# Kernel optimization log

Hardware: AMD Instinct MI355X
Metric: run time of the kernel (lower is better)

Reference implementation:

```python
import jax, jax.numpy as jnp
import numpy as np

N_NODES = 100000
N_EDGES = 1600000
IN_DIM = 16
HEADS = 4
CH = 32  # per-head channels


def _gat_layer(x, src, dst, W, att_src, att_dst, b, concat):
    """PyG GATConv (eval mode): gather -> edge logits -> segment softmax -> scatter-agg."""
    n = x.shape[0]
    H, C = att_src.shape
    h = (x @ W).reshape(n, H, C)                      # [N,H,C]
    a_src = jnp.einsum('nhc,hc->nh', h, att_src)      # [N,H]
    a_dst = jnp.einsum('nhc,hc->nh', h, att_dst)
    e = jax.nn.leaky_relu(a_src[src] + a_dst[dst], negative_slope=0.2)  # [E,H]
    m = jax.ops.segment_max(e, dst, num_segments=n)   # stable softmax per dst node
    p = jnp.exp(e - m[dst])
    s = jax.ops.segment_sum(p, dst, num_segments=n)
    alpha = p / s[dst]                                 # [E,H]
    out = jax.ops.segment_sum(alpha[:, :, None] * h[src], dst, num_segments=n)  # [N,H,C]
    out = out.reshape(n, H * C) if concat else out.mean(axis=1)
    return out + b


def setup_inputs() -> dict:
    key = jax.random.key(0)
    ks = jax.random.split(key, 20)
    d1 = HEADS * CH  # 128

    def gl(k, shape):  # glorot-ish
        fan = sum(shape[-2:]) if len(shape) > 1 else shape[-1]
        return jax.random.normal(k, shape, dtype=jnp.float32) * (2.0 / fan) ** 0.5

    return {
        'x': jax.random.normal(ks[0], (N_NODES, IN_DIM), dtype=jnp.float32),
        'edge_index': jax.random.randint(ks[1], (2, N_EDGES), 0, N_NODES, dtype=jnp.int32),
        'W1': gl(ks[2], (IN_DIM, d1)), 'aS1': gl(ks[3], (HEADS, CH)), 'aD1': gl(ks[4], (HEADS, CH)), 'b1': jnp.zeros((d1,), jnp.float32),
        'W2': gl(ks[5], (d1, d1)),     'aS2': gl(ks[6], (HEADS, CH)), 'aD2': gl(ks[7], (HEADS, CH)), 'b2': jnp.zeros((d1,), jnp.float32),
        'W3': gl(ks[8], (d1, CH)),     'aS3': gl(ks[9], (1, CH)),     'aD3': gl(ks[10], (1, CH)),    'b3': jnp.zeros((CH,), jnp.float32),
        'reg_w': gl(ks[11], (CH, 1)), 'reg_b': jnp.zeros((1,), jnp.float32),
        'cls_w': gl(ks[12], (CH, 1)), 'cls_b': jnp.zeros((1,), jnp.float32),
    }


def reference(x, edge_index, W1, aS1, aD1, b1, W2, aS2, aD2, b2, W3, aS3, aD3, b3, reg_w, reg_b, cls_w, cls_b):
    n = x.shape[0]
    loops = jnp.arange(n, dtype=edge_index.dtype)  # PyG add_self_loops=True
    src = jnp.concatenate([edge_index[0], loops])
    dst = jnp.concatenate([edge_index[1], loops])

    h = jax.nn.elu(_gat_layer(x, src, dst, W1, aS1, aD1, b1, concat=True))
    h = jax.nn.elu(_gat_layer(h, src, dst, W2, aS2, aD2, b2, concat=True)) + h
    h = jax.nn.elu(_gat_layer(h, src, dst, W3, aS3, aD3, b3, concat=False))

    reg = (h @ reg_w + reg_b).squeeze(-1)
    cls = (h @ cls_w + cls_b).squeeze(-1)
    return reg, cls
```

## Files before the change

kernel.cpp:

```cpp
#include <hip/hip_runtime.h>
#include <hip/hip_bf16.h>
#include <cstdint>

#define CDIV(a,b) (((a)+(b)-1)/(b))

__device__ __forceinline__ float lrelu(float x){ return x > 0.f ? x : 0.2f*x; }
__device__ __forceinline__ float eluf(float x){ return x > 0.f ? x : __expf(x) - 1.f; }
__device__ __forceinline__ unsigned short f2bf(float f){
  unsigned x = __float_as_uint(f);
  return (unsigned short)((x + 0x7fffu + ((x >> 16) & 1u)) >> 16);
}
__device__ __forceinline__ float bf2f(unsigned short u){ return __uint_as_float(((unsigned)u) << 16); }

__global__ void hist_k(const int* __restrict__ ei, int* __restrict__ deg, int ne, int etot){
  int e = blockIdx.x*256 + threadIdx.x;
  if (e >= etot) return;
  int d = (e < ne) ? ei[ne + e] : (e - ne);
  atomicAdd(&deg[d], 1);
}

constexpr int SCHUNK = 2048;

__global__ __launch_bounds__(256) void scan_part_k(const int* __restrict__ in, int* __restrict__ out,
                                                   int* __restrict__ blksum, int n){
  __shared__ int lds[256];
  int base = blockIdx.x*SCHUNK + threadIdx.x*8;
  int v[8]; int tsum = 0;
  #pragma unroll
  for (int k=0;k<8;k++){ int idx=base+k; int x=(idx<n)?in[idx]:0; v[k]=tsum; tsum+=x; }
  lds[threadIdx.x]=tsum; __syncthreads();
  for (int off=1; off<256; off<<=1){
    int y = (threadIdx.x>= (unsigned)off)? lds[threadIdx.x-off]:0;
    __syncthreads();
    lds[threadIdx.x]+=y;
    __syncthreads();
  }
  int excl = lds[threadIdx.x] - tsum;
  #pragma unroll
  for (int k=0;k<8;k++){ int idx=base+k; if(idx<n) out[idx]=excl+v[k]; }
  if (threadIdx.x==255) blksum[blockIdx.x]=lds[255];
}

__global__ __launch_bounds__(256) void scan_top_k(int* __restrict__ blksum, int nb){
  __shared__ int lds[256];
  int x = ((int)threadIdx.x<nb)? blksum[threadIdx.x]:0;
  lds[threadIdx.x]=x; __syncthreads();
  for (int off=1; off<256; off<<=1){
    int y=(threadIdx.x>=(unsigned)off)?lds[threadIdx.x-off]:0;
    __syncthreads();
    lds[threadIdx.x]+=y;
    __syncthreads();
  }
  if ((int)threadIdx.x<nb) blksum[threadIdx.x]=lds[threadIdx.x]-x;
}

__global__ void scan_add_k(int* __restrict__ rowstart, const int* __restrict__ blksum,
                           int* __restrict__ cursor, int n, int etot){
  int i = blockIdx.x*256+threadIdx.x;
  if (i<n){ int r = rowstart[i]+blksum[i/SCHUNK]; rowstart[i]=r; cursor[i]=r; }
  if (i==0) rowstart[n]=etot;
}

__global__ void scatter_k(const int* __restrict__ ei, int* __restrict__ cursor,
                          int* __restrict__ edge_src, int ne, int etot, int lo, int hi){
  int e = blockIdx.x*256+threadIdx.x;
  if (e>=etot) return;
  int s,d;
  if (e<ne){ s=ei[e]; d=ei[ne+e]; } else { s=e-ne; d=s; }
  if (d < lo || d >= hi) return;
  int p = atomicAdd(&cursor[d],1);
  edge_src[p]=s;
}

template<int K, int KC, int M, int NPT, int H>
__global__ __launch_bounds__(256) void gemm_att_k(const float* __restrict__ X, const float* __restrict__ W,
    const float* __restrict__ attS, const float* __restrict__ attD,
    unsigned short* __restrict__ Hb, float* __restrict__ asrc, float* __restrict__ adst, int n){
  constexpr int CG = M/8;
  constexpr int NG = 256/CG;
  constexpr int NT = NG*NPT;
  constexpr int XS = KC + 4;
  __shared__ float Xl[NT*XS];
  __shared__ float Wl[KC*M];

  const int tid = threadIdx.x;
  const int cg  = tid % CG;
  const int nd  = tid / CG;
  const int base = blockIdx.x * NT;

  float acc[NPT][8];
  #pragma unroll
  for (int j=0;j<NPT;++j)
    #pragma unroll
    for (int c=0;c<8;++c) acc[j][c]=0.f;

  for (int kc0 = 0; kc0 < K; kc0 += KC){
    __syncthreads();
    for (int i = tid; i < NT*KC/4; i += 256){
      int node = i / (KC/4);
      int k4   = i % (KC/4);
      float4 v = make_float4(0.f,0.f,0.f,0.f);
      if (base + node < n) v = *(const float4*)&X[(size_t)(base+node)*K + kc0 + k4*4];
      *(float4*)&Xl[node*XS + k4*4] = v;
    }
    const float* Wsrc = W + (size_t)kc0*M;
    for (int i = tid; i < KC*M/4; i += 256)
      *(float4*)&Wl[i*4] = *(const float4*)&Wsrc[i*4];
    __syncthreads();

    #pragma unroll 4
    for (int k4 = 0; k4 < KC/4; ++k4){
      float4 xv[NPT];
      #pragma unroll
      for (int j=0;j<NPT;++j) xv[j] = *(const float4*)&Xl[(nd + NG*j)*XS + k4*4];
      #pragma unroll
      for (int kk=0;kk<4;++kk){
        float4 w0 = *(const float4*)&Wl[(k4*4+kk)*M + cg*8];
        float4 w1 = *(const float4*)&Wl[(k4*4+kk)*M + cg*8 + 4];
        #pragma unroll
        for (int j=0;j<NPT;++j){
          float x = ((const float*)&xv[j])[kk];
          acc[j][0] += x*w0.x; acc[j][1] += x*w0.y; acc[j][2] += x*w0.z; acc[j][3] += x*w0.w;
          acc[j][4] += x*w1.x; acc[j][5] += x*w1.y; acc[j][6] += x*w1.z; acc[j][7] += x*w1.w;
        }
      }
    }
  }

  const int c0 = cg*8;
  float s0=attS[c0],s1=attS[c0+1],s2=attS[c0+2],s3=attS[c0+3],
        s4=attS[c0+4],s5=attS[c0+5],s6=attS[c0+6],s7=attS[c0+7];
  float d0=attD[c0],d1=attD[c0+1],d2=attD[c0+2],d3=attD[c0+3],
        d4=attD[c0+4],d5=attD[c0+5],d6=attD[c0+6],d7=attD[c0+7];
  #pragma unroll
  for (int j=0;j<NPT;++j){
    int node = base + nd + NG*j;
    float vs = acc[j][0]*s0+acc[j][1]*s1+acc[j][2]*s2+acc[j][3]*s3
             + acc[j][4]*s4+acc[j][5]*s5+acc[j][6]*s6+acc[j][7]*s7;
    float vd = acc[j][0]*d0+acc[j][1]*d1+acc[j][2]*d2+acc[j][3]*d3
             + acc[j][4]*d4+acc[j][5]*d5+acc[j][6]*d6+acc[j][7]*d7;
    vs += __shfl_xor(vs,1); vs += __shfl_xor(vs,2);
    vd += __shfl_xor(vd,1); vd += __shfl_xor(vd,2);
    if (node < n){
      uint4 pk;
      pk.x = (unsigned)f2bf(acc[j][0]) | ((unsigned)f2bf(acc[j][1])<<16);
      pk.y = (unsigned)f2bf(acc[j][2]) | ((unsigned)f2bf(acc[j][3])<<16);
      pk.z = (unsigned)f2bf(acc[j][4]) | ((unsigned)f2bf(acc[j][5])<<16);
      pk.w = (unsigned)f2bf(acc[j][6]) | ((unsigned)f2bf(acc[j][7])<<16);
      *(uint4*)&Hb[(size_t)node*M + c0] = pk;
      if ((cg & 3)==0){
        int head = cg>>2;
        asrc[(size_t)node*H+head]=vs;
        adst[(size_t)node*H+head]=vd;
      }
    }
  }
}

template<bool RES>
__global__ __launch_bounds__(256, 4) void agg4_k(const unsigned short* __restrict__ Hb, const float* __restrict__ asrc,
    const float* __restrict__ adst, const int* __restrict__ rowstart, const int* __restrict__ esrc,
    const float* __restrict__ bias, float* __restrict__ out, int n){
  __shared__ float alphaS[4][64][4];
  const int w    = threadIdx.x >> 6;
  const int lane = threadIdx.x & 63;
  int wid  = (int)((blockIdx.x*256 + threadIdx.x) >> 6);
  if (wid >= n) return;
  wid = __builtin_amdgcn_readfirstlane(wid);
  const int rs = rowstart[wid], re = rowstart[wid+1];
  const int deg = re - rs;
  const float4 adv = *(const float4*)&adst[(size_t)wid*4];
  const int head = lane >> 4;

  float acc0 = 0.f, acc1 = 0.f;

  if (deg <= 64){
    int s = 0;
    float l0=-1e30f,l1=-1e30f,l2=-1e30f,l3=-1e30f;
    if (lane < deg){
      s = esrc[rs + lane];
      float4 a4 = *(const float4*)&asrc[(size_t)s*4];
      l0 = lrelu(a4.x+adv.x); l1 = lrelu(a4.y+adv.y);
      l2 = lrelu(a4.z+adv.z); l3 = lrelu(a4.w+adv.w);
    }
    float m0=l0,m1=l1,m2=l2,m3=l3;
    #pragma unroll
    for (int mask=32; mask; mask>>=1){
      m0=fmaxf(m0,__shfl_xor(m0,mask)); m1=fmaxf(m1,__shfl_xor(m1,mask));
      m2=fmaxf(m2,__shfl_xor(m2,mask)); m3=fmaxf(m3,__shfl_xor(m3,mask));
    }
    float e0=__expf(l0-m0), e1=__expf(l1-m1), e2=__expf(l2-m2), e3=__expf(l3-m3);
    float s0=e0,s1=e1,s2=e2,s3=e3;
    #pragma unroll
    for (int mask=32; mask; mask>>=1){
      s0+=__shfl_xor(s0,mask); s1+=__shfl_xor(s1,mask);
      s2+=__shfl_xor(s2,mask); s3+=__shfl_xor(s3,mask);
    }
    *(float4*)&alphaS[w][lane][0] = make_float4(e0/s0, e1/s1, e2/s2, e3/s3);

    int jj = 0;
    for (; jj+8 <= deg; jj += 8){
      int sj0 = __builtin_amdgcn_readlane(s, jj+0);
      int sj1 = __builtin_amdgcn_readlane(s, jj+1);
      int sj2 = __builtin_amdgcn_readlane(s, jj+2);
      int sj3 = __builtin_amdgcn_readlane(s, jj+3);
      int sj4 = __builtin_amdgcn_readlane(s, jj+4);
      int sj5 = __builtin_amdgcn_readlane(s, jj+5);
      int sj6 = __builtin_amdgcn_readlane(s, jj+6);
      int sj7 = __builtin_amdgcn_readlane(s, jj+7);
      ushort2 h0 = ((const ushort2*)(Hb + (size_t)sj0*128))[lane];
      ushort2 h1 = ((const ushort2*)(Hb + (size_t)sj1*128))[lane];
      ushort2 h2 = ((const ushort2*)(Hb + (size_t)sj2*128))[lane];
      ushort2 h3 = ((const ushort2*)(Hb + (size_t)sj3*128))[lane];
      ushort2 h4 = ((const ushort2*)(Hb + (size_t)sj4*128))[lane];
      ushort2 h5 = ((const ushort2*)(Hb + (size_t)sj5*128))[lane];
      ushort2 h6 = ((const ushort2*)(Hb + (size_t)sj6*128))[lane];
      ushort2 h7 = ((const ushort2*)(Hb + (size_t)sj7*128))[lane];
      float a0 = alphaS[w][jj+0][head];
      float a1 = alphaS[w][jj+1][head];
      float a2 = alphaS[w][jj+2][head];
      float a3 = alphaS[w][jj+3][head];
      float a4 = alphaS[w][jj+4][head];
      float a5 = alphaS[w][jj+5][head];
      float a6 = alphaS[w][jj+6][head];
      float a7 = alphaS[w][jj+7][head];
      acc0 += a0*bf2f(h0.x) + a1*bf2f(h1.x) + a2*bf2f(h2.x) + a3*bf2f(h3.x)
            + a4*bf2f(h4.x) + a5*bf2f(h5.x) + a6*bf2f(h6.x) + a7*bf2f(h7.x);
      acc1 += a0*bf2f(h0.y) + a1*bf2f(h1.y) + a2*bf2f(h2.y) + a3*bf2f(h3.y)
            + a4*bf2f(h4.y) + a5*bf2f(h5.y) + a6*bf2f(h6.y) + a7*bf2f(h7.y);
    }
    for (; jj+4 <= deg; jj += 4){
      int sj0 = __builtin_amdgcn_readlane(s, jj+0);
      int sj1 = __builtin_amdgcn_readlane(s, jj+1);
      int sj2 = __builtin_amdgcn_readlane(s, jj+2);
      int sj3 = __builtin_amdgcn_readlane(s, jj+3);
      ushort2 h0 = ((const ushort2*)(Hb + (size_t)sj0*128))[lane];
      ushort2 h1 = ((const ushort2*)(Hb + (size_t)sj1*128))[lane];
      ushort2 h2 = ((const ushort2*)(Hb + (size_t)sj2*128))[lane];
      ushort2 h3 = ((const ushort2*)(Hb + (size_t)sj3*128))[lane];
      float a0 = alphaS[w][jj+0][head];
      float a1 = alphaS[w][jj+1][head];
      float a2 = alphaS[w][jj+2][head];
      float a3 = alphaS[w][jj+3][head];
      acc0 += a0*bf2f(h0.x) + a1*bf2f(h1.x) + a2*bf2f(h2.x) + a3*bf2f(h3.x);
      acc1 += a0*bf2f(h0.y) + a1*bf2f(h1.y) + a2*bf2f(h2.y) + a3*bf2f(h3.y);
    }
    for (; jj < deg; ++jj){
      int sj = __builtin_amdgcn_readlane(s, jj);
      ushort2 hv = ((const ushort2*)(Hb + (size_t)sj*128))[lane];
      float a = alphaS[w][jj][head];
      acc0 += a*bf2f(hv.x);
      acc1 += a*bf2f(hv.y);
    }
  } else {
    float adl[4] = {adv.x, adv.y, adv.z, adv.w};
    float m[4] = {-1e30f,-1e30f,-1e30f,-1e30f};
    for (int i = rs + lane; i < re; i += 64){
      int s = esrc[i];
      float4 a4 = *(const float4*)&asrc[(size_t)s*4];
      m[0]=fmaxf(m[0], lrelu(a4.x+adl[0]));
      m[1]=fmaxf(m[1], lrelu(a4.y+adl[1]));
      m[2]=fmaxf(m[2], lrelu(a4.z+adl[2]));
      m[3]=fmaxf(m[3], lrelu(a4.w+adl[3]));
    }
    #pragma unroll
    for (int h=0; h<4; ++h){
      #pragma unroll
      for (int mask=32; mask; mask>>=1) m[h] = fmaxf(m[h], __shfl_xor(m[h], mask));
    }
    float sum[4] = {0.f,0.f,0.f,0.f};
    for (int i = rs + lane; i < re; i += 64){
      int s = esrc[i];
      float4 a4 = *(const float4*)&asrc[(size_t)s*4];
      sum[0]+=__expf(lrelu(a4.x+adl[0])-m[0]);
      sum[1]+=__expf(lrelu(a4.y+adl[1])-m[1]);
      sum[2]+=__expf(lrelu(a4.z+adl[2])-m[2]);
      sum[3]+=__expf(lrelu(a4.w+adl[3])-m[3]);
    }
    #pragma unroll
    for (int h=0; h<4; ++h){
      #pragma unroll
      for (int mask=32; mask; mask>>=1) sum[h]+=__shfl_xor(sum[h],mask);
    }
    const float ad = adl[head], mm = m[head], iv = 1.f/sum[head];
    int i = rs;
    for (; i+4 <= re; i += 4){
      int s0=esrc[i], s1=esrc[i+1], s2=esrc[i+2], s3=esrc[i+3];
      float a0 = asrc[(size_t)s0*4+head];
      float a1 = asrc[(size_t)s1*4+head];
      float a2 = asrc[(size_t)s2*4+head];
      float a3 = asrc[(size_t)s3*4+head];
      ushort2 h0 = ((const ushort2*)(Hb + (size_t)s0*128))[lane];
      ushort2 h1 = ((const ushort2*)(Hb + (size_t)s1*128))[lane];
      ushort2 h2 = ((const ushort2*)(Hb + (size_t)s2*128))[lane];
      ushort2 h3 = ((const ushort2*)(Hb + (size_t)s3*128))[lane];
      float e0=__expf(lrelu(a0+ad)-mm)*iv;
      float e1=__expf(lrelu(a1+ad)-mm)*iv;
      float e2=__expf(lrelu(a2+ad)-mm)*iv;
      float e3=__expf(lrelu(a3+ad)-mm)*iv;
      acc0 += e0*bf2f(h0.x) + e1*bf2f(h1.x) + e2*bf2f(h2.x) + e3*bf2f(h3.x);
      acc1 += e0*bf2f(h0.y) + e1*bf2f(h1.y) + e2*bf2f(h2.y) + e3*bf2f(h3.y);
    }
    for (; i < re; ++i){
      int s = esrc[i];
      float a = asrc[(size_t)s*4+head];
      ushort2 hv = ((const ushort2*)(Hb + (size_t)s*128))[lane];
      float e = __expf(lrelu(a+ad)-mm)*iv;
      acc0 += e*bf2f(hv.x);
      acc1 += e*bf2f(hv.y);
    }
  }

  float2 bv = *(const float2*)&bias[2*lane];
  float v0 = eluf(acc0 + bv.x);
  float v1 = eluf(acc1 + bv.y);
  if (RES){
    float2 rv = *(const float2*)&out[(size_t)wid*128 + 2*lane];
    v0 += rv.x; v1 += rv.y;
  }
  *(float2*)&out[(size_t)wid*128 + 2*lane] = make_float2(v0, v1);
}

__global__ __launch_bounds__(256) void agg1_heads_k(const unsigned short* __restrict__ Hb, const float* __restrict__ asrc,
    const float* __restrict__ adst, const int* __restrict__ rowstart, const int* __restrict__ esrc,
    const float* __restrict__ bias,
    const float* __restrict__ rw, const float* __restrict__ rb,
    const float* __restrict__ cw, const float* __restrict__ cb,
    float* __restrict__ out, int n){
  __shared__ float alphaS[4][64];
  const int w    = threadIdx.x >> 6;
  const int lane = threadIdx.x & 63;
  int wid  = (int)((blockIdx.x*256 + threadIdx.x) >> 6);
  if (wid >= n) return;
  wid = __builtin_amdgcn_readfirstlane(wid);
  const int rs = rowstart[wid], re = rowstart[wid+1];
  const int deg = re - rs;
  const float adl = adst[wid];
  const int q = lane >> 4, c2 = lane & 15;

  float acc0 = 0.f, acc1 = 0.f;

  if (deg <= 64){
    int s = 0;
    float l = -1e30f;
    if (lane < deg){
      s = esrc[rs + lane];
      l = lrelu(asrc[s]+adl);
    }
    float m = l;
    #pragma unroll
    for (int mask=32; mask; mask>>=1) m = fmaxf(m, __shfl_xor(m, mask));
    float e = __expf(l-m);
    float sum = e;
    #pragma unroll
    for (int mask=32; mask; mask>>=1) sum += __shfl_xor(sum, mask);
    alphaS[w][lane] = e/sum;

    for (int jj = 0; jj < deg; jj += 4){
      int idx = jj + q;
      int sj = __shfl(s, idx);
      float av = (idx < 64) ? alphaS[w][idx] : 0.f;
      ushort2 hv = ((const ushort2*)(Hb + (size_t)sj*32))[c2];
      acc0 += av*bf2f(hv.x);
      acc1 += av*bf2f(hv.y);
    }
  } else {
    float m = -1e30f;
    for (int i = rs + lane; i < re; i += 64) m = fmaxf(m, lrelu(asrc[esrc[i]]+adl));
    #pragma unroll
    for (int mask=32; mask; mask>>=1) m = fmaxf(m, __shfl_xor(m, mask));
    float sum = 0.f;
    for (int i = rs + lane; i < re; i += 64) sum += __expf(lrelu(asrc[esrc[i]]+adl)-m);
    #pragma unroll
    for (int mask=32; mask; mask>>=1) sum += __shfl_xor(sum, mask);
    const float iv = 1.f/sum;
    for (int i = rs; i < re; i += 4){
      int eidx = i + q;
      if (eidx < re){
        int s = esrc[eidx];
        float a = asrc[s];
        float e = __expf(lrelu(a+adl)-m)*iv;
        ushort2 hv = ((const ushort2*)(Hb + (size_t)s*32))[c2];
        acc0 += e*bf2f(hv.x);
        acc1 += e*bf2f(hv.y);
      }
    }
  }

  acc0 += __shfl_xor(acc0,16); acc0 += __shfl_xor(acc0,32);
  acc1 += __shfl_xor(acc1,16); acc1 += __shfl_xor(acc1,32);

  float2 bv = *(const float2*)&bias[2*c2];
  float v0 = eluf(acc0 + bv.x);
  float v1 = eluf(acc1 + bv.y);
  float r  = v0*rw[2*c2] + v1*rw[2*c2+1];
  float cl = v0*cw[2*c2] + v1*cw[2*c2+1];
  #pragma unroll
  for (int mask=1; mask<16; mask<<=1){ r += __shfl_xor(r, mask); cl += __shfl_xor(cl, mask); }
  if (lane == 0){
    out[wid]     = r  + rb[0];
    out[n + wid] = cl + cb[0];
  }
}

extern "C" void kernel_launch(void* const* d_in, const int* in_sizes, int n_in,
                              void* d_out, int out_size, void* d_ws, size_t ws_size,
                              hipStream_t stream){
  const float* x   = (const float*)d_in[0];
  const int*   ei  = (const int*)d_in[1];
  const float* W1  = (const float*)d_in[2];
  const float* aS1 = (const float*)d_in[3];
  const float* aD1 = (const float*)d_in[4];
  const float* b1  = (const float*)d_in[5];
  const float* W2  = (const float*)d_in[6];
  const float* aS2 = (const float*)d_in[7];
  const float* aD2 = (const float*)d_in[8];
  const float* b2  = (const float*)d_in[9];
  const float* W3  = (const float*)d_in[10];
  const float* aS3 = (const float*)d_in[11];
  const float* aD3 = (const float*)d_in[12];
  const float* b3  = (const float*)d_in[13];
  const float* rw  = (const float*)d_in[14];
  const float* rb  = (const float*)d_in[15];
  const float* cw  = (const float*)d_in[16];
  const float* cb  = (const float*)d_in[17];
  float* out = (float*)d_out;

  const int n    = in_sizes[0] / 16;
  const int ne   = in_sizes[1] / 2;
  const int etot = ne + n;

  float* A    = (float*)d_ws;
  float* Bf   = A  + (size_t)n*128;
  unsigned short* Hb = (unsigned short*)Bf;
  float* asrc = Bf + (size_t)n*128;
  float* adst = asrc + (size_t)n*4;
  int* deg    = (int*)(adst + (size_t)n*4);
  int* rowst  = deg + n;
  int* cursor = rowst + n + 1;
  int* esrc   = cursor + n;
  int* blksum = esrc + etot;

  hipMemsetAsync(deg, 0, (size_t)n*sizeof(int), stream);
  hist_k<<<CDIV(etot,256),256,0,stream>>>(ei, deg, ne, etot);
  int nblk = CDIV(n, SCHUNK);
  scan_part_k<<<nblk,256,0,stream>>>(deg, rowst, blksum, n);
  scan_top_k<<<1,256,0,stream>>>(blksum, nblk);
  scan_add_k<<<CDIV(n,256),256,0,stream>>>(rowst, blksum, cursor, n, etot);
  for (int p = 0; p < 4; ++p){
    int lo = (int)((size_t)n * p / 4);
    int hi = (int)((size_t)n * (p+1) / 4);
    scatter_k<<<CDIV(etot,256),256,0,stream>>>(ei, cursor, esrc, ne, etot, lo, hi);
  }

  gemm_att_k<16,16,128,4,4><<<CDIV(n,64),256,0,stream>>>(x, W1, aS1, aD1, Hb, asrc, adst, n);
  agg4_k<false><<<CDIV(n,4),256,0,stream>>>(Hb, asrc, adst, rowst, esrc, b1, A, n);

  gemm_att_k<128,32,128,4,4><<<CDIV(n,64),256,0,stream>>>(A, W2, aS2, aD2, Hb, asrc, adst, n);
  agg4_k<true><<<CDIV(n,4),256,0,stream>>>(Hb, asrc, adst, rowst, esrc, b2, A, n);

  gemm_att_k<128,32,32,1,1><<<CDIV(n,64),256,0,stream>>>(A, W3, aS3, aD3, Hb, asrc, adst, n);
  agg1_heads_k<<<CDIV(n,4),256,0,stream>>>(Hb, asrc, adst, rowst, esrc, b3, rw, rb, cw, cb, out, n);
}
```

Measured before the change: 579.4 us.

## Bucket CSR edges by source range within each destination row

The CSR build now counts and scatters edges into 8 sub-buckets per destination node, keyed by the high bits of the source index. Within each row the source indices come out coarsely sorted, so the gathers of source features in the aggregation kernels should hit the cache better. The cost is an 8x larger count and scan array (n*8 ints) plus a longer scan, and it needs n below 8<<14. nblk is about 196, which still fits the single-block top scan.

```diff
diff --git a/kernel.cpp b/kernel.cpp
--- a/kernel.cpp
+++ b/kernel.cpp
@@ -12,22 +12,24 @@
 }
 __device__ __forceinline__ float bf2f(unsigned short u){ return __uint_as_float(((unsigned)u) << 16); }
 
-__global__ void hist_k(const int* __restrict__ ei, int* __restrict__ deg, int ne, int etot){
+constexpr int TSHIFT = 14;
+constexpr int SCH16  = 4096;
+
+__global__ void hist8_k(const int* __restrict__ ei, int* __restrict__ cnt8, int ne, int etot){
   int e = blockIdx.x*256 + threadIdx.x;
   if (e >= etot) return;
-  int d = (e < ne) ? ei[ne + e] : (e - ne);
-  atomicAdd(&deg[d], 1);
-}
-
-constexpr int SCHUNK = 2048;
-
-__global__ __launch_bounds__(256) void scan_part_k(const int* __restrict__ in, int* __restrict__ out,
-                                                   int* __restrict__ blksum, int n){
+  int s,d;
+  if (e<ne){ s=ei[e]; d=ei[ne+e]; } else { s=e-ne; d=s; }
+  atomicAdd(&cnt8[((size_t)d<<3) | (s>>TSHIFT)], 1);
+}
+
+__global__ __launch_bounds__(256) void scan_part16_k(const int* __restrict__ in, int* __restrict__ out,
+                                                     int* __restrict__ blksum, int n){
   __shared__ int lds[256];
-  int base = blockIdx.x*SCHUNK + threadIdx.x*8;
-  int v[8]; int tsum = 0;
+  int base = blockIdx.x*SCH16 + threadIdx.x*16;
+  int v[16]; int tsum = 0;
   #pragma unroll
-  for (int k=0;k<8;k++){ int idx=base+k; int x=(idx<n)?in[idx]:0; v[k]=tsum; tsum+=x; }
+  for (int k=0;k<16;k++){ int idx=base+k; int x=(idx<n)?in[idx]:0; v[k]=tsum; tsum+=x; }
   lds[threadIdx.x]=tsum; __syncthreads();
   for (int off=1; off<256; off<<=1){
     int y = (threadIdx.x>= (unsigned)off)? lds[threadIdx.x-off]:0;
@@ -37,7 +39,7 @@
   }
   int excl = lds[threadIdx.x] - tsum;
   #pragma unroll
-  for (int k=0;k<8;k++){ int idx=base+k; if(idx<n) out[idx]=excl+v[k]; }
+  for (int k=0;k<16;k++){ int idx=base+k; if(idx<n) out[idx]=excl+v[k]; }
   if (threadIdx.x==255) blksum[blockIdx.x]=lds[255];
 }
 
@@ -54,21 +56,25 @@
   if ((int)threadIdx.x<nb) blksum[threadIdx.x]=lds[threadIdx.x]-x;
 }
 
-__global__ void scan_add_k(int* __restrict__ rowstart, const int* __restrict__ blksum,
-                           int* __restrict__ cursor, int n, int etot){
+__global__ void scan_add8_k(int* __restrict__ cursor8, const int* __restrict__ blksum,
+                            int* __restrict__ rowst, int n8, int n, int etot){
   int i = blockIdx.x*256+threadIdx.x;
-  if (i<n){ int r = rowstart[i]+blksum[i/SCHUNK]; rowstart[i]=r; cursor[i]=r; }
-  if (i==0) rowstart[n]=etot;
-}
-
-__global__ void scatter_k(const int* __restrict__ ei, int* __restrict__ cursor,
-                          int* __restrict__ edge_src, int ne, int etot, int lo, int hi){
+  if (i<n8){
+    int r = cursor8[i]+blksum[i/SCH16];
+    cursor8[i]=r;
+    if ((i&7)==0) rowst[i>>3]=r;
+  }
+  if (i==0) rowst[n]=etot;
+}
+
+__global__ void scatter8_k(const int* __restrict__ ei, int* __restrict__ cursor8,
+                           int* __restrict__ edge_src, int ne, int etot, int lo, int hi){
   int e = blockIdx.x*256+threadIdx.x;
   if (e>=etot) return;
   int s,d;
   if (e<ne){ s=ei[e]; d=ei[ne+e]; } else { s=e-ne; d=s; }
   if (d < lo || d >= hi) return;
-  int p = atomicAdd(&cursor[d],1);
+  int p = atomicAdd(&cursor8[((size_t)d<<3) | (s>>TSHIFT)],1);
   edge_src[p]=s;
 }
 
@@ -429,28 +435,29 @@
   const int n    = in_sizes[0] / 16;
   const int ne   = in_sizes[1] / 2;
   const int etot = ne + n;
+  const int n8   = n * 8;
 
   float* A    = (float*)d_ws;
   float* Bf   = A  + (size_t)n*128;
   unsigned short* Hb = (unsigned short*)Bf;
   float* asrc = Bf + (size_t)n*128;
   float* adst = asrc + (size_t)n*4;
-  int* deg    = (int*)(adst + (size_t)n*4);
-  int* rowst  = deg + n;
-  int* cursor = rowst + n + 1;
-  int* esrc   = cursor + n;
+  int* cnt8   = (int*)(adst + (size_t)n*4);
+  int* cursor8= cnt8 + n8;
+  int* rowst  = cursor8 + n8;
+  int* esrc   = rowst + n + 1;
   int* blksum = esrc + etot;
 
-  hipMemsetAsync(deg, 0, (size_t)n*sizeof(int), stream);
-  hist_k<<<CDIV(etot,256),256,0,stream>>>(ei, deg, ne, etot);
-  int nblk = CDIV(n, SCHUNK);
-  scan_part_k<<<nblk,256,0,stream>>>(deg, rowst, blksum, n);
+  hipMemsetAsync(cnt8, 0, (size_t)n8*sizeof(int), stream);
+  hist8_k<<<CDIV(etot,256),256,0,stream>>>(ei, cnt8, ne, etot);
+  int nblk = CDIV(n8, SCH16);
+  scan_part16_k<<<nblk,256,0,stream>>>(cnt8, cursor8, blksum, n8);
   scan_top_k<<<1,256,0,stream>>>(blksum, nblk);
-  scan_add_k<<<CDIV(n,256),256,0,stream>>>(rowst, blksum, cursor, n, etot);
+  scan_add8_k<<<CDIV(n8,256),256,0,stream>>>(cursor8, blksum, rowst, n8, n, etot);
   for (int p = 0; p < 4; ++p){
     int lo = (int)((size_t)n * p / 4);
     int hi = (int)((size_t)n * (p+1) / 4);
-    scatter_k<<<CDIV(etot,256),256,0,stream>>>(ei, cursor, esrc, ne, etot, lo, hi);
+    scatter8_k<<<CDIV(etot,256),256,0,stream>>>(ei, cursor8, esrc, ne, etot, lo, hi);
   }
 
   gemm_att_k<16,16,128,4,4><<<CDIV(n,64),256,0,stream>>>(x, W1, aS1, aD1, Hb, asrc, adst, n);
```

Result: slower. 592.3 us (+2.2%).
